# Kernel tuning notes

Measured on AMD Instinct MI355X. Metric: run time of the kernel, lower is better.

Reference implementation:

```python
import jax, jax.numpy as jnp
import numpy as np

N_ = 50000   # nodes
E_ = 800000  # edges
G_ = 64      # graphs in batch
EPS = 1e-5   # batchnorm eps


def _lin(k, fi, fo):
    s = 1.0 / np.sqrt(fi)
    return jax.random.uniform(k, (fi, fo), jnp.float32, -s, s)


def setup_inputs() -> dict:
    key = jax.random.key(0)
    ks = jax.random.split(key, 16)
    d_in, d_h, d_out = 128, 128, 5000
    inp = {
        'x': jax.random.normal(ks[0], (N_, d_in), jnp.float32),
        'edge_index': jax.random.randint(ks[1], (2, E_), 0, N_, jnp.int32),
        'batch': jnp.sort(jax.random.randint(ks[2], (N_,), 0, G_, jnp.int32)),
    }
    dims = [(d_in, d_h), (d_h, d_h), (d_h, d_h), (d_h, d_h)]
    for i, (fi, fo) in enumerate(dims, 1):
        inp[f'w{i}'] = _lin(ks[2 + i], fi, fo)
        inp[f'b{i}'] = jnp.zeros((fo,), jnp.float32)
        inp[f'g{i}'] = jnp.ones((fo,), jnp.float32)   # BN gamma
        inp[f'be{i}'] = jnp.zeros((fo,), jnp.float32)  # BN beta
    inp['gw1'] = _lin(ks[7], d_h, d_h // 2)
    inp['gb1'] = jnp.zeros((d_h // 2,), jnp.float32)
    inp['gw2'] = _lin(ks[8], d_h // 2, 1)
    inp['gb2'] = jnp.zeros((1,), jnp.float32)
    inp['cw'] = _lin(ks[9], d_h, d_out)
    inp['cb'] = jnp.zeros((d_out,), jnp.float32)
    return inp


def reference(x, w1, b1, g1, be1, w2, b2, g2, be2, w3, b3, g3, be3,
              w4, b4, g4, be4, gw1, gb1, gw2, gb2, cw, cb,
              edge_index, batch):
    # GCN normalization with self-loops (PyG GCNConv semantics)
    loops = jnp.arange(N_, dtype=edge_index.dtype)
    src = jnp.concatenate([edge_index[0], loops])
    dst = jnp.concatenate([edge_index[1], loops])
    deg = jax.ops.segment_sum(jnp.ones(src.shape[0], jnp.float32), dst, N_)
    dis = jax.lax.rsqrt(jnp.maximum(deg, 1.0))  # deg >= 1 with self-loops
    norm = dis[src] * dis[dst]                  # [E+N]

    def gcn(h, w, b):
        hw = h @ w                              # [N, d]
        msg = hw[src] * norm[:, None]           # gather over edges
        return jax.ops.segment_sum(msg, dst, N_) + b

    def bn(h, g, be):
        m = h.mean(0)
        v = h.var(0)                            # biased var (training BN)
        return (h - m) * jax.lax.rsqrt(v + EPS) * g + be

    h = x
    for w, b, g, be in ((w1, b1, g1, be1), (w2, b2, g2, be2),
                        (w3, b3, g3, be3), (w4, b4, g4, be4)):
        h = jax.nn.relu(bn(gcn(h, w, b), g, be))  # dropout is identity (eval)

    # attention pooling: per-graph softmax over gate scores
    gate = jax.nn.relu(h @ gw1 + gb1) @ gw2 + gb2  # [N, 1]
    gate = gate[:, 0]
    m = jax.ops.segment_max(gate, batch, G_)
    e = jnp.exp(gate - m[batch])
    s = jax.ops.segment_sum(e, batch, G_)
    a = e / s[batch]                               # [N]
    pooled = jax.ops.segment_sum(h * a[:, None], batch, G_)  # [G, d]
    return pooled @ cw + cb                        # [G, out]
```

## Files before the change

### kernel.cpp

```cpp
#include <hip/hip_runtime.h>
#include <hip/hip_bf16.h>
#include <hip/hip_fp16.h>

#define NN   50000
#define NE   800000
#define NG   64
#define DH   128
#define DOUT 5000
#define BNEPS 1e-5f
#define NBLK 196

typedef _Float16 h8 __attribute__((ext_vector_type(8)));
typedef float    f4 __attribute__((ext_vector_type(4)));

__global__ __launch_bounds__(256) void k_count(const int* __restrict__ dst, int* __restrict__ cnt) {
    int e = blockIdx.x * 256 + threadIdx.x;
    if (e < NE) atomicAdd(&cnt[dst[e]], 1);
}

__global__ __launch_bounds__(256) void k_blkscan(const int* __restrict__ cnt, int* __restrict__ rowptr,
                                                 int* __restrict__ bsum) {
    __shared__ int s[256];
    int t = threadIdx.x, i = blockIdx.x * 256 + t;
    int v = (i < NN) ? cnt[i] : 0;
    s[t] = v;
    __syncthreads();
    for (int off = 1; off < 256; off <<= 1) {
        int x = (t >= off) ? s[t - off] : 0;
        __syncthreads();
        s[t] += x;
        __syncthreads();
    }
    if (i < NN) rowptr[i] = s[t] - v;
    if (t == 255) bsum[blockIdx.x] = s[255];
}

__global__ __launch_bounds__(256) void k_bscan(const int* __restrict__ bsum, int* __restrict__ boff) {
    __shared__ int s[256];
    int t = threadIdx.x;
    int v = (t < NBLK) ? bsum[t] : 0;
    s[t] = v;
    __syncthreads();
    for (int off = 1; off < 256; off <<= 1) {
        int x = (t >= off) ? s[t - off] : 0;
        __syncthreads();
        s[t] += x;
        __syncthreads();
    }
    if (t < NBLK) boff[t] = s[t] - v;
}

__global__ __launch_bounds__(256) void k_fin(int* __restrict__ rowptr, const int* __restrict__ boff,
                                             int* __restrict__ cnt, float* __restrict__ dis) {
    int i = blockIdx.x * 256 + threadIdx.x;
    if (i >= NN) { if (i == NN) rowptr[NN] = NE; return; }
    rowptr[i] += boff[blockIdx.x];
    dis[i] = rsqrtf((float)(cnt[i] + 1));
    cnt[i] = 0;
}

__global__ __launch_bounds__(256) void k_fill(const int* __restrict__ ei, const int* __restrict__ rowptr,
                                              int* __restrict__ fil, const float* __restrict__ dis,
                                              int2* __restrict__ ew) {
    int e = blockIdx.x * 256 + threadIdx.x;
    if (e >= NE) return;
    int s = ei[e], d = ei[NE + e];
    int p = rowptr[d] + atomicAdd(&fil[d], 1);
    ew[p] = make_int2(s, __float_as_int(dis[s] * dis[d]));
}

__global__ __launch_bounds__(256) void k_wprep(const float* __restrict__ W0, const float* __restrict__ W1,
                                               const float* __restrict__ W2, const float* __restrict__ W3,
                                               __half* __restrict__ Wt) {
    const float* Ws[4] = {W0, W1, W2, W3};
    int m = blockIdx.x >> 4;
    int chunk = blockIdx.x & 15;
    const float* W = Ws[m];
    __half* O = Wt + m * DH * DH;
    int o = chunk * 1024 + threadIdx.x;
    for (int r = 0; r < 4; r++, o += 256) {
        int c = o >> 7, k = o & 127;
        O[o] = __float2half(W[k * DH + c]);
    }
}

__global__ __launch_bounds__(256) void k_gemm3(const float* __restrict__ X, const __half* __restrict__ Wt,
                                               const float* __restrict__ scale, const float* __restrict__ shift,
                                               __half* __restrict__ Y) {
    int t = threadIdx.x;
    int lane = t & 63, wid = t >> 6;
    int wr = wid >> 1, wc = wid & 1;
    int row0 = blockIdx.x * 64;
    int lr = lane & 15, lk = (lane >> 4) * 8;

    f4 acc[2][4];
#pragma unroll
    for (int i = 0; i < 2; i++)
#pragma unroll
        for (int j = 0; j < 4; j++) acc[i][j] = (f4){0.f, 0.f, 0.f, 0.f};

    for (int kt = 0; kt < 4; kt++) {
        int kbase = kt * 32 + lk;
        h8 afr[2];
#pragma unroll
        for (int fr = 0; fr < 2; fr++) {
            int gr = row0 + wr * 32 + fr * 16 + lr;
            gr = min(gr, NN - 1);
            const float4* p = (const float4*)(X + (size_t)gr * DH + kbase);
            float4 v0 = p[0], v1 = p[1];
            if (scale) {
                const float4* sc4 = (const float4*)(scale + kbase);
                const float4* sh4 = (const float4*)(shift + kbase);
                float4 s0 = sc4[0], s1 = sc4[1], h0 = sh4[0], h1 = sh4[1];
                v0.x = fmaxf(fmaf(v0.x, s0.x, h0.x), 0.f);
                v0.y = fmaxf(fmaf(v0.y, s0.y, h0.y), 0.f);
                v0.z = fmaxf(fmaf(v0.z, s0.z, h0.z), 0.f);
                v0.w = fmaxf(fmaf(v0.w, s0.w, h0.w), 0.f);
                v1.x = fmaxf(fmaf(v1.x, s1.x, h1.x), 0.f);
                v1.y = fmaxf(fmaf(v1.y, s1.y, h1.y), 0.f);
                v1.z = fmaxf(fmaf(v1.z, s1.z, h1.z), 0.f);
                v1.w = fmaxf(fmaf(v1.w, s1.w, h1.w), 0.f);
            }
            h8 a;
            a[0] = (_Float16)v0.x; a[1] = (_Float16)v0.y; a[2] = (_Float16)v0.z; a[3] = (_Float16)v0.w;
            a[4] = (_Float16)v1.x; a[5] = (_Float16)v1.y; a[6] = (_Float16)v1.z; a[7] = (_Float16)v1.w;
            afr[fr] = a;
        }
#pragma unroll
        for (int fc = 0; fc < 4; fc++) {
            int gc = wc * 64 + fc * 16 + lr;
            h8 b = *(const h8*)(Wt + (size_t)gc * DH + kbase);
#pragma unroll
            for (int fr = 0; fr < 2; fr++)
                acc[fr][fc] = __builtin_amdgcn_mfma_f32_16x16x32_f16(afr[fr], b, acc[fr][fc], 0, 0, 0);
        }
    }
#pragma unroll
    for (int fr = 0; fr < 2; fr++) {
#pragma unroll
        for (int fc = 0; fc < 4; fc++) {
            int C = wc * 64 + fc * 16 + lr;
#pragma unroll
            for (int q = 0; q < 4; q++) {
                int R = row0 + wr * 32 + fr * 16 + (lane >> 4) * 4 + q;
                if (R < NN) Y[(size_t)R * DH + C] = __float2half(acc[fr][fc][q]);
            }
        }
    }
}

#define EDGE(e) { int2 r = HW4[(size_t)(e).x * 32 + sl]; \
                  float w = __int_as_float((e).y); \
                  float2 g0 = __half22float2(*(__half2*)&r.x), g1 = __half22float2(*(__half2*)&r.y); \
                  a0 = fmaf(w, g0.x, a0); a1 = fmaf(w, g0.y, a1); \
                  a2 = fmaf(w, g1.x, a2); a3 = fmaf(w, g1.y, a3); }

__global__ __launch_bounds__(256) void k_agg(const __half* __restrict__ HW, const int* __restrict__ rowptr,
                                             const int2* __restrict__ EW, const float* __restrict__ dis,
                                             const float* __restrict__ bias, float* __restrict__ OUT,
                                             float* __restrict__ ssum, float* __restrict__ ssq) {
    __shared__ float lsum[DH], lsq[DH];
    int t = threadIdx.x;
    if (t < DH) { lsum[t] = 0.f; lsq[t] = 0.f; }
    __syncthreads();
    int wid = t >> 6, lane = t & 63;
    int sub = lane >> 5, sl = lane & 31;
    const int2* HW4 = (const int2*)HW;
    float4* OUT4 = (float4*)OUT;
    float4 bv = ((const float4*)bias)[sl];
    float s0 = 0, s1 = 0, s2 = 0, s3 = 0, q0 = 0, q1 = 0, q2 = 0, q3 = 0;
    int gw = blockIdx.x * 4 + wid;
    for (int i = gw * 2 + sub; i < NN; i += 16384) {
        float sd = dis[i];
        int2 hr = HW4[(size_t)i * 32 + sl];
        float2 f0 = __half22float2(*(__half2*)&hr.x);
        float2 f1 = __half22float2(*(__half2*)&hr.y);
        float wslf = sd * sd;
        float a0 = wslf * f0.x, a1 = wslf * f0.y;
        float a2 = wslf * f1.x, a3 = wslf * f1.y;
        int p = rowptr[i], p1 = rowptr[i + 1];
        for (; p + 8 <= p1; p += 8) {
            int2 e0 = EW[p], e1 = EW[p + 1], e2 = EW[p + 2], e3 = EW[p + 3];
            int2 e4 = EW[p + 4], e5 = EW[p + 5], e6 = EW[p + 6], e7 = EW[p + 7];
            EDGE(e0) EDGE(e1) EDGE(e2) EDGE(e3)
            EDGE(e4) EDGE(e5) EDGE(e6) EDGE(e7)
        }
        if (p + 4 <= p1) {
            int2 e0 = EW[p], e1 = EW[p + 1], e2 = EW[p + 2], e3 = EW[p + 3];
            EDGE(e0) EDGE(e1) EDGE(e2) EDGE(e3)
            p += 4;
        }
        for (; p < p1; p++) {
            int2 e = EW[p];
            EDGE(e)
        }
        a0 += bv.x; a1 += bv.y; a2 += bv.z; a3 += bv.w;
        OUT4[(size_t)i * 32 + sl] = make_float4(a0, a1, a2, a3);
        s0 += a0; s1 += a1; s2 += a2; s3 += a3;
        q0 += a0 * a0; q1 += a1 * a1; q2 += a2 * a2; q3 += a3 * a3;
    }
    atomicAdd(&lsum[sl * 4 + 0], s0); atomicAdd(&lsum[sl * 4 + 1], s1);
    atomicAdd(&lsum[sl * 4 + 2], s2); atomicAdd(&lsum[sl * 4 + 3], s3);
    atomicAdd(&lsq[sl * 4 + 0], q0);  atomicAdd(&lsq[sl * 4 + 1], q1);
    atomicAdd(&lsq[sl * 4 + 2], q2);  atomicAdd(&lsq[sl * 4 + 3], q3);
    __syncthreads();
    if (t < DH) { atomicAdd(&ssum[t], lsum[t]); atomicAdd(&ssq[t], lsq[t]); }
}

__global__ void k_bnfin(float* __restrict__ ssum, float* __restrict__ ssq,
                        const float* __restrict__ g, const float* __restrict__ be,
                        float* __restrict__ scale, float* __restrict__ shift) {
    int f = threadIdx.x;
    float m = ssum[f] * (1.f / NN);
    float v = ssq[f] * (1.f / NN) - m * m;
    float r = rsqrtf(v + BNEPS);
    float sc = r * g[f];
    scale[f] = sc;
    shift[f] = fmaf(-m, sc, be[f]);
    ssum[f] = 0.f;
    ssq[f] = 0.f;
}

__global__ __launch_bounds__(256) void k_gate(const float* __restrict__ H, const float* __restrict__ scale,
                                              const float* __restrict__ shift, const float* __restrict__ gw1,
                                              const float* __restrict__ gb1, const float* __restrict__ gw2,
                                              const float* __restrict__ gb2, float* __restrict__ gate) {
    __shared__ float w1s[DH * 64];
    __shared__ float rowbuf[4][DH];
    int t = threadIdx.x;
    for (int i = t; i < DH * 64; i += 256) w1s[i] = gw1[i];
    __syncthreads();
    int wid = t >> 6, lane = t & 63;
    float b1v = gb1[lane], w2v = gw2[lane], b2v = gb2[0];
    float2 sc2 = ((const float2*)scale)[lane];
    float2 sh2 = ((const float2*)shift)[lane];
    int nw = gridDim.x * 4;
    int iters = (NN + nw - 1) / nw;
    const float2* H2 = (const float2*)H;
    for (int it = 0; it < iters; it++) {
        int i = blockIdx.x * 4 + wid + it * nw;
        bool act = i < NN;
        if (act) {
            float2 hv = H2[i * 64 + lane];
            rowbuf[wid][lane * 2] = fmaxf(fmaf(hv.x, sc2.x, sh2.x), 0.f);
            rowbuf[wid][lane * 2 + 1] = fmaxf(fmaf(hv.y, sc2.y, sh2.y), 0.f);
        }
        __syncthreads();
        float hid = 0.f;
#pragma unroll 8
        for (int k = 0; k < DH; k++) hid = fmaf(rowbuf[wid][k], w1s[k * 64 + lane], hid);
        hid = fmaxf(hid + b1v, 0.f);
        float v = hid * w2v;
        for (int off = 32; off > 0; off >>= 1) v += __shfl_down(v, off, 64);
        if (act && lane == 0) gate[i] = v + b2v;
        __syncthreads();
    }
}

__device__ __forceinline__ int lbound(const int* __restrict__ a, int v) {
    int lo = 0, hi = NN;
    while (lo < hi) {
        int mid = (lo + hi) >> 1;
        if (a[mid] < v) lo = mid + 1; else hi = mid;
    }
    return lo;
}

__global__ __launch_bounds__(256) void k_pms(const float* __restrict__ gate, const int* __restrict__ batch,
                                             float* __restrict__ ms, float* __restrict__ pooled) {
    __shared__ float red[256];
    int g = blockIdx.x, t = threadIdx.x;
    if (t < DH) pooled[g * DH + t] = 0.f;
    int s = lbound(batch, g), e = lbound(batch, g + 1);
    float m = -INFINITY;
    for (int i = s + t; i < e; i += 256) m = fmaxf(m, gate[i]);
    red[t] = m; __syncthreads();
    for (int off = 128; off > 0; off >>= 1) { if (t < off) red[t] = fmaxf(red[t], red[t + off]); __syncthreads(); }
    m = red[0];
    __syncthreads();
    float se = 0.f;
    for (int i = s + t; i < e; i += 256) se += __expf(gate[i] - m);
    red[t] = se; __syncthreads();
    for (int off = 128; off > 0; off >>= 1) { if (t < off) red[t] += red[t + off]; __syncthreads(); }
    if (t == 0) {
        ms[g * 2] = m;
        ms[g * 2 + 1] = (e > s) ? 1.f / red[0] : 0.f;
    }
}

#define PNODES 8
__global__ __launch_bounds__(256) void k_pool2(const float* __restrict__ H, const float* __restrict__ scale,
                                               const float* __restrict__ shift, const float* __restrict__ gate,
                                               const int* __restrict__ batch, const float* __restrict__ ms,
                                               float* __restrict__ pooled) {
    int wid = threadIdx.x >> 6, lane = threadIdx.x & 63;
    int base = (blockIdx.x * 4 + wid) * PNODES;
    if (base >= NN) return;
    int end = min(base + PNODES, NN);
    const float2* H2 = (const float2*)H;
    float2 sc2 = ((const float2*)scale)[lane];
    float2 sh2 = ((const float2*)shift)[lane];
    float2 acc = make_float2(0.f, 0.f);
    int curg = batch[base];
    for (int i = base; i < end; i++) {
        int g = batch[i];
        if (g != curg) {
            atomicAdd(&pooled[curg * DH + lane * 2], acc.x);
            atomicAdd(&pooled[curg * DH + lane * 2 + 1], acc.y);
            acc = make_float2(0.f, 0.f);
            curg = g;
        }
        float a = __expf(gate[i] - ms[g * 2]) * ms[g * 2 + 1];
        float2 h = H2[i * 64 + lane];
        float hx = fmaxf(fmaf(h.x, sc2.x, sh2.x), 0.f);
        float hy = fmaxf(fmaf(h.y, sc2.y, sh2.y), 0.f);
        acc.x = fmaf(a, hx, acc.x);
        acc.y = fmaf(a, hy, acc.y);
    }
    atomicAdd(&pooled[curg * DH + lane * 2], acc.x);
    atomicAdd(&pooled[curg * DH + lane * 2 + 1], acc.y);
}

__global__ __launch_bounds__(256) void k_cls(const float* __restrict__ pooled, const float* __restrict__ cw,
                                             const float* __restrict__ cb, float* __restrict__ out) {
    __shared__ float pr[DH];
    int g = blockIdx.y;
    if (threadIdx.x < DH) pr[threadIdx.x] = pooled[g * DH + threadIdx.x];
    __syncthreads();
    int j = blockIdx.x * 256 + threadIdx.x;
    if (j >= DOUT) return;
    float acc = cb[j];
#pragma unroll 8
    for (int k = 0; k < DH; k++) acc = fmaf(pr[k], cw[k * DOUT + j], acc);
    out[g * DOUT + j] = acc;
}

extern "C" void kernel_launch(void* const* d_in, const int* in_sizes, int n_in,
                              void* d_out, int out_size, void* d_ws, size_t ws_size,
                              hipStream_t stream) {
    const float* x     = (const float*)d_in[0];
    const int*   ei    = (const int*)d_in[1];
    const int*   batch = (const int*)d_in[2];
    const float* w[4]  = {(const float*)d_in[3], (const float*)d_in[7], (const float*)d_in[11], (const float*)d_in[15]};
    const float* bb[4] = {(const float*)d_in[4], (const float*)d_in[8], (const float*)d_in[12], (const float*)d_in[16]};
    const float* gg[4] = {(const float*)d_in[5], (const float*)d_in[9], (const float*)d_in[13], (const float*)d_in[17]};
    const float* be[4] = {(const float*)d_in[6], (const float*)d_in[10], (const float*)d_in[14], (const float*)d_in[18]};
    const float* gw1 = (const float*)d_in[19];
    const float* gb1 = (const float*)d_in[20];
    const float* gw2 = (const float*)d_in[21];
    const float* gb2 = (const float*)d_in[22];
    const float* cw  = (const float*)d_in[23];
    const float* cb  = (const float*)d_in[24];

    char* base = (char*)d_ws;
    size_t off = 0;
    auto take = [&](size_t n) -> char* { char* r = base + off; off = (off + n + 255) & ~(size_t)255; return r; };
    float*  bufA   = (float*)take((size_t)NN * DH * 4);
    __half* bufB   = (__half*)take((size_t)NN * DH * 2);
    int2*  ew     = (int2*)take((size_t)NE * 8);
    int*   rowptr = (int*)take((size_t)(NN + 1) * 4);
    int*   cnt    = (int*)take((size_t)NN * 4);
    float* dis    = (float*)take((size_t)NN * 4);
    float* gate   = (float*)take((size_t)NN * 4);
    float* stats  = (float*)take(2 * DH * 4);
    float* ssum = stats, *ssq = stats + DH;
    float* scale  = (float*)take(DH * 4);
    float* shift  = (float*)take(DH * 4);
    float* pooled = (float*)take((size_t)NG * DH * 4);
    int*   bsum   = (int*)take((size_t)256 * 4);
    int*   boff   = (int*)take((size_t)256 * 4);
    float* ms     = (float*)take((size_t)NG * 2 * 4);
    __half* Wt    = (__half*)take((size_t)4 * DH * DH * 2);

    hipMemsetAsync(cnt, 0, NN * 4, stream);
    hipMemsetAsync(stats, 0, 2 * DH * 4, stream);
    k_count<<<(NE + 255) / 256, 256, 0, stream>>>(ei + NE, cnt);
    k_blkscan<<<NBLK, 256, 0, stream>>>(cnt, rowptr, bsum);
    k_bscan<<<1, 256, 0, stream>>>(bsum, boff);
    k_fin<<<NBLK, 256, 0, stream>>>(rowptr, boff, cnt, dis);
    k_fill<<<(NE + 255) / 256, 256, 0, stream>>>(ei, rowptr, cnt, dis, ew);
    k_wprep<<<64, 256, 0, stream>>>(w[0], w[1], w[2], w[3], Wt);

    const int gemm_grid = (NN + 63) / 64;
    for (int L = 0; L < 4; L++) {
        k_gemm3<<<gemm_grid, 256, 0, stream>>>(L == 0 ? x : bufA, Wt + (size_t)L * DH * DH,
                                               L == 0 ? nullptr : scale,
                                               L == 0 ? nullptr : shift, bufB);
        k_agg<<<2048, 256, 0, stream>>>(bufB, rowptr, ew, dis, bb[L], bufA, ssum, ssq);
        k_bnfin<<<1, DH, 0, stream>>>(ssum, ssq, gg[L], be[L], scale, shift);
    }
    k_gate<<<1024, 256, 0, stream>>>(bufA, scale, shift, gw1, gb1, gw2, gb2, gate);
    k_pms<<<NG, 256, 0, stream>>>(gate, batch, ms, pooled);
    k_pool2<<<(NN + 4 * PNODES - 1) / (4 * PNODES), 256, 0, stream>>>(bufA, scale, shift, gate, batch, ms, pooled);
    k_cls<<<dim3((DOUT + 255) / 256, NG), 256, 0, stream>>>(pooled, cw, cb, (float*)d_out);
}
```

Before: 594.7 us.

## Store aggregated activations in fp16, drop bias add, use nontemporal edge loads

The aggregation output buffer changes from fp32 to fp16. This halves the write traffic in k_agg and the read traffic in the next GEMM, the gate kernel and the pooling kernel, with the GEMM gaining a half-input path. The GCN bias add is removed, since training-mode batchnorm subtracts the per-feature mean and cancels any constant bias. Edge-list loads and the output stores use nontemporal hints so they do not evict the gathered feature rows from cache. The cost is reduced precision in the intermediate activations.

```diff
diff --git a/kernel.cpp b/kernel.cpp
--- a/kernel.cpp
+++ b/kernel.cpp
@@ -12,6 +12,11 @@
 
 typedef _Float16 h8 __attribute__((ext_vector_type(8)));
 typedef float    f4 __attribute__((ext_vector_type(4)));
+
+__device__ __forceinline__ int2 ntload2(const int2* p) {
+    long long v = __builtin_nontemporal_load((const long long*)p);
+    int2 r; r.x = (int)(unsigned)(v & 0xffffffffLL); r.y = (int)(v >> 32); return r;
+}
 
 __global__ __launch_bounds__(256) void k_count(const int* __restrict__ dst, int* __restrict__ cnt) {
     int e = blockIdx.x * 256 + threadIdx.x;
@@ -84,7 +89,8 @@
     }
 }
 
-__global__ __launch_bounds__(256) void k_gemm3(const float* __restrict__ X, const __half* __restrict__ Wt,
+__global__ __launch_bounds__(256) void k_gemm3(const float* __restrict__ Xf, const __half* __restrict__ Xh,
+                                               const __half* __restrict__ Wt,
                                                const float* __restrict__ scale, const float* __restrict__ shift,
                                                __half* __restrict__ Y) {
     int t = threadIdx.x;
@@ -106,24 +112,31 @@
         for (int fr = 0; fr < 2; fr++) {
             int gr = row0 + wr * 32 + fr * 16 + lr;
             gr = min(gr, NN - 1);
-            const float4* p = (const float4*)(X + (size_t)gr * DH + kbase);
-            float4 v0 = p[0], v1 = p[1];
-            if (scale) {
+            float fv[8];
+            if (Xf) {
+                const float4* p = (const float4*)(Xf + (size_t)gr * DH + kbase);
+                float4 v0 = p[0], v1 = p[1];
+                fv[0] = v0.x; fv[1] = v0.y; fv[2] = v0.z; fv[3] = v0.w;
+                fv[4] = v1.x; fv[5] = v1.y; fv[6] = v1.z; fv[7] = v1.w;
+            } else {
+                int4 hv = *(const int4*)(Xh + (size_t)gr * DH + kbase);
+                float2 p0 = __half22float2(*(__half2*)&hv.x);
+                float2 p1 = __half22float2(*(__half2*)&hv.y);
+                float2 p2 = __half22float2(*(__half2*)&hv.z);
+                float2 p3 = __half22float2(*(__half2*)&hv.w);
+                fv[0] = p0.x; fv[1] = p0.y; fv[2] = p1.x; fv[3] = p1.y;
+                fv[4] = p2.x; fv[5] = p2.y; fv[6] = p3.x; fv[7] = p3.y;
                 const float4* sc4 = (const float4*)(scale + kbase);
                 const float4* sh4 = (const float4*)(shift + kbase);
                 float4 s0 = sc4[0], s1 = sc4[1], h0 = sh4[0], h1 = sh4[1];
-                v0.x = fmaxf(fmaf(v0.x, s0.x, h0.x), 0.f);
-                v0.y = fmaxf(fmaf(v0.y, s0.y, h0.y), 0.f);
-                v0.z = fmaxf(fmaf(v0.z, s0.z, h0.z), 0.f);
-                v0.w = fmaxf(fmaf(v0.w, s0.w, h0.w), 0.f);
-                v1.x = fmaxf(fmaf(v1.x, s1.x, h1.x), 0.f);
-                v1.y = fmaxf(fmaf(v1.y, s1.y, h1.y), 0.f);
-                v1.z = fmaxf(fmaf(v1.z, s1.z, h1.z), 0.f);
-                v1.w = fmaxf(fmaf(v1.w, s1.w, h1.w), 0.f);
+                float sv[8] = {s0.x, s0.y, s0.z, s0.w, s1.x, s1.y, s1.z, s1.w};
+                float hv2[8] = {h0.x, h0.y, h0.z, h0.w, h1.x, h1.y, h1.z, h1.w};
+#pragma unroll
+                for (int j = 0; j < 8; j++) fv[j] = fmaxf(fmaf(fv[j], sv[j], hv2[j]), 0.f);
             }
             h8 a;
-            a[0] = (_Float16)v0.x; a[1] = (_Float16)v0.y; a[2] = (_Float16)v0.z; a[3] = (_Float16)v0.w;
-            a[4] = (_Float16)v1.x; a[5] = (_Float16)v1.y; a[6] = (_Float16)v1.z; a[7] = (_Float16)v1.w;
+#pragma unroll
+            for (int j = 0; j < 8; j++) a[j] = (_Float16)fv[j];
             afr[fr] = a;
         }
 #pragma unroll
@@ -157,7 +170,7 @@
 
 __global__ __launch_bounds__(256) void k_agg(const __half* __restrict__ HW, const int* __restrict__ rowptr,
                                              const int2* __restrict__ EW, const float* __restrict__ dis,
-                                             const float* __restrict__ bias, float* __restrict__ OUT,
+                                             __half* __restrict__ OUT,
                                              float* __restrict__ ssum, float* __restrict__ ssq) {
     __shared__ float lsum[DH], lsq[DH];
     int t = threadIdx.x;
@@ -166,8 +179,6 @@
     int wid = t >> 6, lane = t & 63;
     int sub = lane >> 5, sl = lane & 31;
     const int2* HW4 = (const int2*)HW;
-    float4* OUT4 = (float4*)OUT;
-    float4 bv = ((const float4*)bias)[sl];
     float s0 = 0, s1 = 0, s2 = 0, s3 = 0, q0 = 0, q1 = 0, q2 = 0, q3 = 0;
     int gw = blockIdx.x * 4 + wid;
     for (int i = gw * 2 + sub; i < NN; i += 16384) {
@@ -180,22 +191,28 @@
         float a2 = wslf * f1.x, a3 = wslf * f1.y;
         int p = rowptr[i], p1 = rowptr[i + 1];
         for (; p + 8 <= p1; p += 8) {
-            int2 e0 = EW[p], e1 = EW[p + 1], e2 = EW[p + 2], e3 = EW[p + 3];
-            int2 e4 = EW[p + 4], e5 = EW[p + 5], e6 = EW[p + 6], e7 = EW[p + 7];
+            int2 e0 = ntload2(EW + p),     e1 = ntload2(EW + p + 1);
+            int2 e2 = ntload2(EW + p + 2), e3 = ntload2(EW + p + 3);
+            int2 e4 = ntload2(EW + p + 4), e5 = ntload2(EW + p + 5);
+            int2 e6 = ntload2(EW + p + 6), e7 = ntload2(EW + p + 7);
             EDGE(e0) EDGE(e1) EDGE(e2) EDGE(e3)
             EDGE(e4) EDGE(e5) EDGE(e6) EDGE(e7)
         }
         if (p + 4 <= p1) {
-            int2 e0 = EW[p], e1 = EW[p + 1], e2 = EW[p + 2], e3 = EW[p + 3];
+            int2 e0 = ntload2(EW + p),     e1 = ntload2(EW + p + 1);
+            int2 e2 = ntload2(EW + p + 2), e3 = ntload2(EW + p + 3);
             EDGE(e0) EDGE(e1) EDGE(e2) EDGE(e3)
             p += 4;
         }
         for (; p < p1; p++) {
-            int2 e = EW[p];
+            int2 e = ntload2(EW + p);
             EDGE(e)
         }
-        a0 += bv.x; a1 += bv.y; a2 += bv.z; a3 += bv.w;
-        OUT4[(size_t)i * 32 + sl] = make_float4(a0, a1, a2, a3);
+        __half2 o01 = __floats2half2_rn(a0, a1);
+        __half2 o23 = __floats2half2_rn(a2, a3);
+        int i01 = *(int*)&o01, i23 = *(int*)&o23;
+        long long ov = ((long long)(unsigned)i23 << 32) | (unsigned)i01;
+        __builtin_nontemporal_store(ov, (long long*)(OUT + (size_t)i * DH + sl * 4));
         s0 += a0; s1 += a1; s2 += a2; s3 += a3;
         q0 += a0 * a0; q1 += a1 * a1; q2 += a2 * a2; q3 += a3 * a3;
     }
@@ -221,7 +238,7 @@
     ssq[f] = 0.f;
 }
 
-__global__ __launch_bounds__(256) void k_gate(const float* __restrict__ H, const float* __restrict__ scale,
+__global__ __launch_bounds__(256) void k_gate(const __half* __restrict__ H, const float* __restrict__ scale,
                                               const float* __restrict__ shift, const float* __restrict__ gw1,
                                               const float* __restrict__ gb1, const float* __restrict__ gw2,
                                               const float* __restrict__ gb2, float* __restrict__ gate) {
@@ -236,12 +253,12 @@
     float2 sh2 = ((const float2*)shift)[lane];
     int nw = gridDim.x * 4;
     int iters = (NN + nw - 1) / nw;
-    const float2* H2 = (const float2*)H;
+    const __half2* H2 = (const __half2*)H;
     for (int it = 0; it < iters; it++) {
         int i = blockIdx.x * 4 + wid + it * nw;
         bool act = i < NN;
         if (act) {
-            float2 hv = H2[i * 64 + lane];
+            float2 hv = __half22float2(H2[(size_t)i * 64 + lane]);
             rowbuf[wid][lane * 2] = fmaxf(fmaf(hv.x, sc2.x, sh2.x), 0.f);
             rowbuf[wid][lane * 2 + 1] = fmaxf(fmaf(hv.y, sc2.y, sh2.y), 0.f);
         }
@@ -289,7 +306,7 @@
 }
 
 #define PNODES 8
-__global__ __launch_bounds__(256) void k_pool2(const float* __restrict__ H, const float* __restrict__ scale,
+__global__ __launch_bounds__(256) void k_pool2(const __half* __restrict__ H, const float* __restrict__ scale,
                                                const float* __restrict__ shift, const float* __restrict__ gate,
                                                const int* __restrict__ batch, const float* __restrict__ ms,
                                                float* __restrict__ pooled) {
@@ -297,7 +314,7 @@
     int base = (blockIdx.x * 4 + wid) * PNODES;
     if (base >= NN) return;
     int end = min(base + PNODES, NN);
-    const float2* H2 = (const float2*)H;
+    const __half2* H2 = (const __half2*)H;
     float2 sc2 = ((const float2*)scale)[lane];
     float2 sh2 = ((const float2*)shift)[lane];
     float2 acc = make_float2(0.f, 0.f);
@@ -311,7 +328,7 @@
             curg = g;
         }
         float a = __expf(gate[i] - ms[g * 2]) * ms[g * 2 + 1];
-        float2 h = H2[i * 64 + lane];
+        float2 h = __half22float2(H2[(size_t)i * 64 + lane]);
         float hx = fmaxf(fmaf(h.x, sc2.x, sh2.x), 0.f);
         float hy = fmaxf(fmaf(h.y, sc2.y, sh2.y), 0.f);
         acc.x = fmaf(a, hx, acc.x);
@@ -342,7 +359,6 @@
     const int*   ei    = (const int*)d_in[1];
     const int*   batch = (const int*)d_in[2];
     const float* w[4]  = {(const float*)d_in[3], (const float*)d_in[7], (const float*)d_in[11], (const float*)d_in[15]};
-    const float* bb[4] = {(const float*)d_in[4], (const float*)d_in[8], (const float*)d_in[12], (const float*)d_in[16]};
     const float* gg[4] = {(const float*)d_in[5], (const float*)d_in[9], (const float*)d_in[13], (const float*)d_in[17]};
     const float* be[4] = {(const float*)d_in[6], (const float*)d_in[10], (const float*)d_in[14], (const float*)d_in[18]};
     const float* gw1 = (const float*)d_in[19];
@@ -355,7 +371,7 @@
     char* base = (char*)d_ws;
     size_t off = 0;
     auto take = [&](size_t n) -> char* { char* r = base + off; off = (off + n + 255) & ~(size_t)255; return r; };
-    float*  bufA   = (float*)take((size_t)NN * DH * 4);
+    __half* bufA   = (__half*)take((size_t)NN * DH * 2);
     __half* bufB   = (__half*)take((size_t)NN * DH * 2);
     int2*  ew     = (int2*)take((size_t)NE * 8);
     int*   rowptr = (int*)take((size_t)(NN + 1) * 4);
@@ -383,10 +399,11 @@
 
     const int gemm_grid = (NN + 63) / 64;
     for (int L = 0; L < 4; L++) {
-        k_gemm3<<<gemm_grid, 256, 0, stream>>>(L == 0 ? x : bufA, Wt + (size_t)L * DH * DH,
+        k_gemm3<<<gemm_grid, 256, 0, stream>>>(L == 0 ? x : nullptr, L == 0 ? nullptr : bufA,
+                                               Wt + (size_t)L * DH * DH,
                                                L == 0 ? nullptr : scale,
                                                L == 0 ? nullptr : shift, bufB);
-        k_agg<<<2048, 256, 0, stream>>>(bufB, rowptr, ew, dis, bb[L], bufA, ssum, ssq);
+        k_agg<<<2048, 256, 0, stream>>>(bufB, rowptr, ew, dis, bufA, ssum, ssq);
         k_bnfin<<<1, DH, 0, stream>>>(ssum, ssq, gg[L], be[L], scale, shift);
     }
     k_gate<<<1024, 256, 0, stream>>>(bufA, scale, shift, gw1, gb1, gw2, gb2, gate);
```

New measurement: 621.4 us. 1.04x slower.

## Compute attention gate MLP with fp16 MFMA and drop bias add before BN

Applied to the files above, without the earlier changes.

Replaces the scalar LDS-based gate MLP kernel with an MFMA kernel that applies BN+ReLU on load, converts activations to fp16 and multiplies by a pre-transposed fp16 copy of gw1, made by the extended weight prep kernel. The GCN bias add is removed from aggregation because a per-feature constant is cancelled by the following batch-norm mean subtraction. The gate gets fp16 input precision in exchange for fewer scalar FMAs and less shared memory traffic.

```diff
diff --git a/kernel.cpp b/kernel.cpp
--- a/kernel.cpp
+++ b/kernel.cpp
@@ -71,16 +71,20 @@
 
 __global__ __launch_bounds__(256) void k_wprep(const float* __restrict__ W0, const float* __restrict__ W1,
                                                const float* __restrict__ W2, const float* __restrict__ W3,
-                                               __half* __restrict__ Wt) {
-    const float* Ws[4] = {W0, W1, W2, W3};
+                                               const float* __restrict__ GW1, __half* __restrict__ Wt) {
+    const float* Ws[5] = {W0, W1, W2, W3, GW1};
     int m = blockIdx.x >> 4;
     int chunk = blockIdx.x & 15;
     const float* W = Ws[m];
     __half* O = Wt + m * DH * DH;
+    int ncol = (m == 4) ? 64 : DH;
+    int total = ncol * DH;
     int o = chunk * 1024 + threadIdx.x;
     for (int r = 0; r < 4; r++, o += 256) {
-        int c = o >> 7, k = o & 127;
-        O[o] = __float2half(W[k * DH + c]);
+        if (o < total) {
+            int c = o >> 7, k = o & 127;
+            O[o] = __float2half(W[k * ncol + c]);
+        }
     }
 }
 
@@ -157,7 +161,7 @@
 
 __global__ __launch_bounds__(256) void k_agg(const __half* __restrict__ HW, const int* __restrict__ rowptr,
                                              const int2* __restrict__ EW, const float* __restrict__ dis,
-                                             const float* __restrict__ bias, float* __restrict__ OUT,
+                                             float* __restrict__ OUT,
                                              float* __restrict__ ssum, float* __restrict__ ssq) {
     __shared__ float lsum[DH], lsq[DH];
     int t = threadIdx.x;
@@ -167,7 +171,6 @@
     int sub = lane >> 5, sl = lane & 31;
     const int2* HW4 = (const int2*)HW;
     float4* OUT4 = (float4*)OUT;
-    float4 bv = ((const float4*)bias)[sl];
     float s0 = 0, s1 = 0, s2 = 0, s3 = 0, q0 = 0, q1 = 0, q2 = 0, q3 = 0;
     int gw = blockIdx.x * 4 + wid;
     for (int i = gw * 2 + sub; i < NN; i += 16384) {
@@ -194,7 +197,6 @@
             int2 e = EW[p];
             EDGE(e)
         }
-        a0 += bv.x; a1 += bv.y; a2 += bv.z; a3 += bv.w;
         OUT4[(size_t)i * 32 + sl] = make_float4(a0, a1, a2, a3);
         s0 += a0; s1 += a1; s2 += a2; s3 += a3;
         q0 += a0 * a0; q1 += a1 * a1; q2 += a2 * a2; q3 += a3 * a3;
@@ -221,39 +223,62 @@
     ssq[f] = 0.f;
 }
 
-__global__ __launch_bounds__(256) void k_gate(const float* __restrict__ H, const float* __restrict__ scale,
-                                              const float* __restrict__ shift, const float* __restrict__ gw1,
-                                              const float* __restrict__ gb1, const float* __restrict__ gw2,
-                                              const float* __restrict__ gb2, float* __restrict__ gate) {
-    __shared__ float w1s[DH * 64];
-    __shared__ float rowbuf[4][DH];
-    int t = threadIdx.x;
-    for (int i = t; i < DH * 64; i += 256) w1s[i] = gw1[i];
-    __syncthreads();
-    int wid = t >> 6, lane = t & 63;
-    float b1v = gb1[lane], w2v = gw2[lane], b2v = gb2[0];
-    float2 sc2 = ((const float2*)scale)[lane];
-    float2 sh2 = ((const float2*)shift)[lane];
-    int nw = gridDim.x * 4;
-    int iters = (NN + nw - 1) / nw;
-    const float2* H2 = (const float2*)H;
-    for (int it = 0; it < iters; it++) {
-        int i = blockIdx.x * 4 + wid + it * nw;
-        bool act = i < NN;
-        if (act) {
-            float2 hv = H2[i * 64 + lane];
-            rowbuf[wid][lane * 2] = fmaxf(fmaf(hv.x, sc2.x, sh2.x), 0.f);
-            rowbuf[wid][lane * 2 + 1] = fmaxf(fmaf(hv.y, sc2.y, sh2.y), 0.f);
-        }
-        __syncthreads();
-        float hid = 0.f;
-#pragma unroll 8
-        for (int k = 0; k < DH; k++) hid = fmaf(rowbuf[wid][k], w1s[k * 64 + lane], hid);
-        hid = fmaxf(hid + b1v, 0.f);
-        float v = hid * w2v;
-        for (int off = 32; off > 0; off >>= 1) v += __shfl_down(v, off, 64);
-        if (act && lane == 0) gate[i] = v + b2v;
-        __syncthreads();
+__global__ __launch_bounds__(256) void k_gateM(const float* __restrict__ H, const float* __restrict__ scale,
+                                               const float* __restrict__ shift, const __half* __restrict__ gw1t,
+                                               const float* __restrict__ gb1, const float* __restrict__ gw2,
+                                               const float* __restrict__ gb2, float* __restrict__ gate) {
+    int t = threadIdx.x, lane = t & 63, w = t >> 6;
+    int row0 = blockIdx.x * 64 + w * 16;
+    int lr = lane & 15, lk = (lane >> 4) * 8;
+    f4 acc[4];
+#pragma unroll
+    for (int fc = 0; fc < 4; fc++) acc[fc] = (f4){0.f, 0.f, 0.f, 0.f};
+
+    for (int kt = 0; kt < 4; kt++) {
+        int kbase = kt * 32 + lk;
+        int gr = min(row0 + lr, NN - 1);
+        const float4* p = (const float4*)(H + (size_t)gr * DH + kbase);
+        float4 v0 = p[0], v1 = p[1];
+        const float4* sc4 = (const float4*)(scale + kbase);
+        const float4* sh4 = (const float4*)(shift + kbase);
+        float4 s0 = sc4[0], s1 = sc4[1], h0 = sh4[0], h1 = sh4[1];
+        v0.x = fmaxf(fmaf(v0.x, s0.x, h0.x), 0.f);
+        v0.y = fmaxf(fmaf(v0.y, s0.y, h0.y), 0.f);
+        v0.z = fmaxf(fmaf(v0.z, s0.z, h0.z), 0.f);
+        v0.w = fmaxf(fmaf(v0.w, s0.w, h0.w), 0.f);
+        v1.x = fmaxf(fmaf(v1.x, s1.x, h1.x), 0.f);
+        v1.y = fmaxf(fmaf(v1.y, s1.y, h1.y), 0.f);
+        v1.z = fmaxf(fmaf(v1.z, s1.z, h1.z), 0.f);
+        v1.w = fmaxf(fmaf(v1.w, s1.w, h1.w), 0.f);
+        h8 a;
+        a[0] = (_Float16)v0.x; a[1] = (_Float16)v0.y; a[2] = (_Float16)v0.z; a[3] = (_Float16)v0.w;
+        a[4] = (_Float16)v1.x; a[5] = (_Float16)v1.y; a[6] = (_Float16)v1.z; a[7] = (_Float16)v1.w;
+#pragma unroll
+        for (int fc = 0; fc < 4; fc++) {
+            h8 b = *(const h8*)(gw1t + (size_t)(fc * 16 + lr) * DH + kbase);
+            acc[fc] = __builtin_amdgcn_mfma_f32_16x16x32_f16(a, b, acc[fc], 0, 0, 0);
+        }
+    }
+    float vq[4] = {0.f, 0.f, 0.f, 0.f};
+#pragma unroll
+    for (int fc = 0; fc < 4; fc++) {
+        float b1 = gb1[fc * 16 + lr];
+        float w2 = gw2[fc * 16 + lr];
+#pragma unroll
+        for (int q = 0; q < 4; q++)
+            vq[q] = fmaf(fmaxf(acc[fc][q] + b1, 0.f), w2, vq[q]);
+    }
+#pragma unroll
+    for (int m = 1; m < 16; m <<= 1) {
+#pragma unroll
+        for (int q = 0; q < 4; q++) vq[q] += __shfl_xor(vq[q], m, 64);
+    }
+    if (lr == 0) {
+        float b2 = gb2[0];
+        int rbase = row0 + (lane >> 4) * 4;
+#pragma unroll
+        for (int q = 0; q < 4; q++)
+            if (rbase + q < NN) gate[rbase + q] = vq[q] + b2;
     }
 }
 
@@ -311,7 +336,7 @@
             curg = g;
         }
         float a = __expf(gate[i] - ms[g * 2]) * ms[g * 2 + 1];
-        float2 h = H2[i * 64 + lane];
+        float2 h = H2[(size_t)i * 64 + lane];
         float hx = fmaxf(fmaf(h.x, sc2.x, sh2.x), 0.f);
         float hy = fmaxf(fmaf(h.y, sc2.y, sh2.y), 0.f);
         acc.x = fmaf(a, hx, acc.x);
@@ -342,7 +367,6 @@
     const int*   ei    = (const int*)d_in[1];
     const int*   batch = (const int*)d_in[2];
     const float* w[4]  = {(const float*)d_in[3], (const float*)d_in[7], (const float*)d_in[11], (const float*)d_in[15]};
-    const float* bb[4] = {(const float*)d_in[4], (const float*)d_in[8], (const float*)d_in[12], (const float*)d_in[16]};
     const float* gg[4] = {(const float*)d_in[5], (const float*)d_in[9], (const float*)d_in[13], (const float*)d_in[17]};
     const float* be[4] = {(const float*)d_in[6], (const float*)d_in[10], (const float*)d_in[14], (const float*)d_in[18]};
     const float* gw1 = (const float*)d_in[19];
@@ -370,7 +394,8 @@
     int*   bsum   = (int*)take((size_t)256 * 4);
     int*   boff   = (int*)take((size_t)256 * 4);
     float* ms     = (float*)take((size_t)NG * 2 * 4);
-    __half* Wt    = (__half*)take((size_t)4 * DH * DH * 2);
+    __half* Wt    = (__half*)take((size_t)5 * DH * DH * 2);
+    __half* gw1t  = Wt + (size_t)4 * DH * DH;
 
     hipMemsetAsync(cnt, 0, NN * 4, stream);
     hipMemsetAsync(stats, 0, 2 * DH * 4, stream);
@@ -379,17 +404,17 @@
     k_bscan<<<1, 256, 0, stream>>>(bsum, boff);
     k_fin<<<NBLK, 256, 0, stream>>>(rowptr, boff, cnt, dis);
     k_fill<<<(NE + 255) / 256, 256, 0, stream>>>(ei, rowptr, cnt, dis, ew);
-    k_wprep<<<64, 256, 0, stream>>>(w[0], w[1], w[2], w[3], Wt);
+    k_wprep<<<72, 256, 0, stream>>>(w[0], w[1], w[2], w[3], gw1, Wt);
 
     const int gemm_grid = (NN + 63) / 64;
     for (int L = 0; L < 4; L++) {
         k_gemm3<<<gemm_grid, 256, 0, stream>>>(L == 0 ? x : bufA, Wt + (size_t)L * DH * DH,
                                                L == 0 ? nullptr : scale,
                                                L == 0 ? nullptr : shift, bufB);
-        k_agg<<<2048, 256, 0, stream>>>(bufB, rowptr, ew, dis, bb[L], bufA, ssum, ssq);
+        k_agg<<<2048, 256, 0, stream>>>(bufB, rowptr, ew, dis, bufA, ssum, ssq);
         k_bnfin<<<1, DH, 0, stream>>>(ssum, ssq, gg[L], be[L], scale, shift);
     }
-    k_gate<<<1024, 256, 0, stream>>>(bufA, scale, shift, gw1, gb1, gw2, gb2, gate);
+    k_gateM<<<(NN + 63) / 64, 256, 0, stream>>>(bufA, scale, shift, gw1t, gb1, gw2, gb2, gate);
     k_pms<<<NG, 256, 0, stream>>>(gate, batch, ms, pooled);
     k_pool2<<<(NN + 4 * PNODES - 1) / (4 * PNODES), 256, 0, stream>>>(bufA, scale, shift, gate, batch, ms, pooled);
     k_cls<<<dim3((DOUT + 255) / 256, NG), 256, 0, stream>>>(pooled, cw, cb, (float*)d_out);
```

After: 584.3 us. Within noise of the previous version (-1.7%).
